# Performance work log

Measured on AMD Instinct MI355X. Metric: run time of the kernel, lower is better.

## Reference

```python
import jax, jax.numpy as jnp
import numpy as np

B, S, H, W, DF, D, HID, ITERS = 8, 8, 64, 64, 64, 64, 128, 3
EPS = 1e-8


def build_grid(h, w):
    ranges = [np.linspace(-1.0, 1.0, num=h), np.linspace(-1.0, 1.0, num=w)]
    g = np.meshgrid(*ranges, sparse=False, indexing='xy')
    return jnp.asarray(np.stack(g, axis=-1), dtype=jnp.float32)  # [H, W, 2]


def ln(x, g, b):
    m = jnp.mean(x, axis=-1, keepdims=True)
    v = jnp.mean((x - m) ** 2, axis=-1, keepdims=True)
    return (x - m) * jax.lax.rsqrt(v + 1e-5) * g + b


def setup_inputs() -> dict:
    key = jax.random.key(0)
    ks = iter(jax.random.split(key, 64))
    def nrm(shape, s=0.02):
        return jax.random.normal(next(ks), shape, jnp.float32) * s
    inp = {}
    inp['inputs'] = jax.random.normal(next(ks), (B, H, W, DF), jnp.float32)
    # learned slot inits and learned per-slot position / scale factors
    inp['slots_p'] = jax.random.normal(next(ks), (1, S, D), jnp.float32)
    inp['s_pos_p'] = 2.0 * jax.random.uniform(next(ks), (1, S, 2), jnp.float32) - 1.0
    inp['s_scale_p'] = 0.1 + 0.01 * jax.random.normal(next(ks), (1, S, 2), jnp.float32)
    # soft position embedding Linear(2, D)
    inp['W_pos'] = nrm((2, D)); inp['b_pos'] = jnp.zeros((D,), jnp.float32)
    # q/k/v projections
    inp['Wq'] = nrm((D, D)); inp['bq'] = jnp.zeros((D,), jnp.float32)
    inp['Wk'] = nrm((DF, D)); inp['bk'] = jnp.zeros((D,), jnp.float32)
    inp['Wv'] = nrm((DF, D)); inp['bv'] = jnp.zeros((D,), jnp.float32)
    # layernorms
    inp['g_in'] = jnp.ones((DF,), jnp.float32); inp['b_in'] = jnp.zeros((DF,), jnp.float32)
    inp['g_slots'] = jnp.ones((D,), jnp.float32); inp['b_slots'] = jnp.zeros((D,), jnp.float32)
    inp['g_k'] = jnp.ones((D,), jnp.float32); inp['b_k'] = jnp.zeros((D,), jnp.float32)
    inp['g_v'] = jnp.ones((D,), jnp.float32); inp['b_v'] = jnp.zeros((D,), jnp.float32)
    # shared kv MLP fc1_kv / fc2_kv
    inp['W1'] = nrm((D, 2 * D)); inp['b1'] = jnp.zeros((2 * D,), jnp.float32)
    inp['W2'] = nrm((2 * D, D)); inp['b2'] = jnp.zeros((D,), jnp.float32)
    # GRUCell (torch layout transposed to [in, 3*D])
    inp['W_ih'] = nrm((D, 3 * D)); inp['b_ih'] = jnp.zeros((3 * D,), jnp.float32)
    inp['W_hh'] = nrm((D, 3 * D)); inp['b_hh'] = jnp.zeros((3 * D,), jnp.float32)
    # residual slot MLP
    inp['g_pre'] = jnp.ones((D,), jnp.float32); inp['b_pre'] = jnp.zeros((D,), jnp.float32)
    inp['Wf1'] = nrm((D, HID)); inp['bf1'] = jnp.zeros((HID,), jnp.float32)
    inp['Wf2'] = nrm((HID, D)); inp['bf2'] = jnp.zeros((D,), jnp.float32)
    return inp


def reference(inputs, slots_p, s_pos_p, s_scale_p, W_pos, b_pos, Wq, bq, Wk, bk, Wv, bv,
              g_in, b_in, g_slots, b_slots, g_k, b_k, g_v, b_v, W1, b1, W2, b2,
              W_ih, W_hh, b_ih, b_hh, g_pre, b_pre, Wf1, bf1, Wf2, bf2):
    grid = build_grid(H, W)                 # [H, W, 2]
    grid_flat = grid.reshape(-1, 2)          # [HW, 2]
    scale = D ** (-0.5)

    x = ln(inputs, g_in, b_in)
    k0 = x @ Wk + bk                         # [B, H, W, D]
    v0 = x @ Wv + bv

    slots = jnp.broadcast_to(slots_p, (B, S, D))
    s_pos = jnp.clip(jnp.broadcast_to(s_pos_p, (B, S, 2)), -1.0, 1.0)[:, :, None, None, :]
    s_scale = jnp.clip(jnp.broadcast_to(s_scale_p, (B, S, 2)), 1e-3, 2.0)[:, :, None, None, :]

    def proj_kv(base, sp, ss, g, b):
        gr = (grid[None, None] - sp) / (ss * 5.0)      # [B, S, H, W, 2]
        pe = gr @ W_pos + b_pos                        # [B, S, H, W, D]
        t = (base[:, None] + pe).reshape(B, S, H * W, D)
        t = ln(t, g, b)
        return jax.nn.relu(t @ W1 + b1) @ W2 + b2      # [B, S, HW, D]

    for i in range(ITERS + 1):
        slots_prev = slots
        q = ln(slots, g_slots, b_slots) @ Wq + bq       # [B, S, D]
        kk = proj_kv(k0, s_pos, s_scale, g_k, b_k)
        vv = proj_kv(v0, s_pos, s_scale, g_v, b_v)
        dots = jnp.einsum('bid,bijd->bij', q, kk) * scale
        attn_mask = jax.nn.softmax(dots, axis=1) + EPS  # softmax over slot axis
        attn = attn_mask / jnp.sum(attn_mask, axis=-1, keepdims=True)
        updates = jnp.einsum('bijd,bij->bid', vv, attn)
        if i < ITERS:
            xg = updates.reshape(-1, D) @ W_ih + b_ih
            hg = slots_prev.reshape(-1, D) @ W_hh + b_hh
            ir, iz, inn = jnp.split(xg, 3, axis=-1)
            hr, hz, hn = jnp.split(hg, 3, axis=-1)
            r = jax.nn.sigmoid(ir + hr)
            z = jax.nn.sigmoid(iz + hz)
            n = jnp.tanh(inn + r * hn)
            slots = ((1.0 - z) * n + z * slots_prev.reshape(-1, D)).reshape(B, S, D)
            slots = slots + (jax.nn.relu(ln(slots, g_pre, b_pre) @ Wf1 + bf1) @ Wf2 + bf2)
        else:
            slots = slots_prev
        # update per-slot position / scale from the attention mask
        sp = jnp.einsum('bij,jd->bid', attn_mask, grid_flat) / jnp.sum(attn_mask, axis=-1, keepdims=True)
        diff = grid_flat[None, None] - sp[:, :, None]   # [B, S, HW, 2]
        am = attn_mask + 1e-8
        ss = jnp.sqrt(jnp.einsum('bij,bijd->bid', am, diff ** 2) / jnp.sum(am, axis=-1, keepdims=True))
        s_pos = sp[:, :, None, None, :]
        s_scale = jnp.clip(ss, 1e-3, 2.0)[:, :, None, None, :]
    return slots, s_pos, s_scale, attn_mask
```

## Files before the change

kernel.cpp:

```cpp
#include <hip/hip_runtime.h>
#include <math.h>

typedef __bf16 bf16_t;
typedef __bf16 bfrag __attribute__((ext_vector_type(8)));
typedef float ffrag __attribute__((ext_vector_type(4)));

__device__ __forceinline__ float wave_sum(float v) {
#pragma unroll
  for (int m = 32; m >= 1; m >>= 1) v += __shfl_xor(v, m, 64);
  return v;
}
__device__ __forceinline__ float lin_(int i) { return -1.f + (2.f * (float)i) / 63.f; }
__device__ __forceinline__ float bflo(unsigned u) { return __uint_as_float(u << 16); }
__device__ __forceinline__ float bfhi(unsigned u) { return __uint_as_float(u & 0xFFFF0000u); }

__device__ __forceinline__ void pass_type(
    const bf16_t xs[][72], bf16_t t0s[][72],
    const bf16_t WTl[][72], const bf16_t W1l[][72],
    const float* __restrict__ bias, const float* wpxs, const float* wpys,
    const float* bpvs, float* __restrict__ statsG, bf16_t* __restrict__ P0G,
    int j0, int wv, int lq, int ln15) {
  ffrag C[4] = {{0,0,0,0},{0,0,0,0},{0,0,0,0},{0,0,0,0}};
#pragma unroll
  for (int ks = 0; ks < 2; ++ks) {
    bfrag a = *(const bfrag*)&xs[wv * 16 + ln15][ks * 32 + lq * 8];
#pragma unroll
    for (int nt = 0; nt < 4; ++nt) {
      bfrag bb = *(const bfrag*)&WTl[nt * 16 + ln15][ks * 32 + lq * 8];
      C[nt] = __builtin_amdgcn_mfma_f32_16x16x32_bf16(a, bb, C[nt], 0, 0, 0);
    }
  }
  float kv[4][4];
  float st[5][4];
#pragma unroll
  for (int i = 0; i < 5; ++i)
#pragma unroll
    for (int rg = 0; rg < 4; ++rg) st[i][rg] = 0.f;
#pragma unroll
  for (int nt = 0; nt < 4; ++nt) {
    int n = nt * 16 + ln15;
    float bn = bias[n], pxw = wpxs[n], pyw = wpys[n], bpw = bpvs[n];
#pragma unroll
    for (int rg = 0; rg < 4; ++rg) {
      float v = C[nt][rg] + bn;
      kv[nt][rg] = v;
      st[0][rg] += v; st[1][rg] += v * v; st[2][rg] += v * pxw;
      st[3][rg] += v * pyw; st[4][rg] += v * bpw;
    }
  }
#pragma unroll
  for (int i = 0; i < 5; ++i)
#pragma unroll
    for (int rg = 0; rg < 4; ++rg) {
      float v = st[i][rg];
      v += __shfl_xor(v, 1, 64); v += __shfl_xor(v, 2, 64);
      v += __shfl_xor(v, 4, 64); v += __shfl_xor(v, 8, 64);
      st[i][rg] = v;
    }
  if (ln15 == 0) {
#pragma unroll
    for (int rg = 0; rg < 4; ++rg) {
      int j = j0 + wv * 16 + lq * 4 + rg;
#pragma unroll
      for (int i = 0; i < 5; ++i) statsG[j * 5 + i] = st[i][rg];
    }
  }
#pragma unroll
  for (int nt = 0; nt < 4; ++nt)
#pragma unroll
    for (int rg = 0; rg < 4; ++rg)
      t0s[wv * 16 + lq * 4 + rg][nt * 16 + ln15] = (bf16_t)kv[nt][rg];
  ffrag D[8] = {{0,0,0,0},{0,0,0,0},{0,0,0,0},{0,0,0,0},
                {0,0,0,0},{0,0,0,0},{0,0,0,0},{0,0,0,0}};
#pragma unroll
  for (int ks = 0; ks < 2; ++ks) {
    bfrag a = *(const bfrag*)&t0s[wv * 16 + ln15][ks * 32 + lq * 8];
#pragma unroll
    for (int nt = 0; nt < 8; ++nt) {
      bfrag bb = *(const bfrag*)&W1l[nt * 16 + ln15][ks * 32 + lq * 8];
      D[nt] = __builtin_amdgcn_mfma_f32_16x16x32_bf16(a, bb, D[nt], 0, 0, 0);
    }
  }
#pragma unroll
  for (int nt = 0; nt < 8; ++nt)
#pragma unroll
    for (int rg = 0; rg < 4; ++rg)
      P0G[(size_t)(j0 + wv * 16 + lq * 4 + rg) * 128 + nt * 16 + ln15] =
          (bf16_t)D[nt][rg];
}

__global__ __launch_bounds__(256) void k_pre(
    const float* __restrict__ inp, const float* __restrict__ g_in,
    const float* __restrict__ b_in, const float* __restrict__ bk,
    const float* __restrict__ bv, const float* __restrict__ Wk,
    const float* __restrict__ Wv, const float* __restrict__ W1,
    const float* __restrict__ g_k, const float* __restrict__ g_v,
    const float* __restrict__ W_pos, const float* __restrict__ b_pos,
    bf16_t* __restrict__ P0k, bf16_t* __restrict__ P0v,
    float* __restrict__ statsK, float* __restrict__ statsV,
    const float* __restrict__ slots_p, const float* __restrict__ g_slots,
    const float* __restrict__ b_slots, const float* __restrict__ Wq,
    const float* __restrict__ bq, const float* __restrict__ W2,
    const float* __restrict__ b2, float* __restrict__ w2qg,
    float* __restrict__ b2qg,
    const float* __restrict__ b_k, const float* __restrict__ b_v,
    const float* __restrict__ b1, const float* __restrict__ s_pos_p,
    const float* __restrict__ s_scale_p,
    float4* __restrict__ nckA, float* __restrict__ nckB,
    float4* __restrict__ ncvA, float* __restrict__ ncvB,
    float* __restrict__ possum, float* __restrict__ sposS,
    float* __restrict__ sscaleS, float* __restrict__ slotsS) {
  __shared__ bf16_t xs[64][72];
  __shared__ bf16_t t0s[64][72];
  __shared__ bf16_t WkTl[64][72];
  __shared__ bf16_t WvTl[64][72];
  __shared__ bf16_t W1kl[128][72];
  __shared__ bf16_t W1vl[128][72];
  __shared__ float wpxs[64], wpys[64], bpvs[64];
  const int tid = threadIdx.x;
  const int j0 = blockIdx.x * 64;
  for (int i = tid; i < 4096; i += 256) {
    int n = i & 63, d = i >> 6;
    WkTl[n][d] = (bf16_t)Wk[i];
    WvTl[n][d] = (bf16_t)Wv[i];
  }
  for (int i = tid; i < 8192; i += 256) {
    int n = i & 127, c = i >> 7;
    float w = W1[i];
    W1kl[n][c] = (bf16_t)(g_k[c] * w);
    W1vl[n][c] = (bf16_t)(g_v[c] * w);
  }
  if (tid < 64) { wpxs[tid] = W_pos[tid]; wpys[tid] = W_pos[64 + tid]; bpvs[tid] = b_pos[tid]; }
  {
    const int px = tid >> 2, cg = tid & 3;
    const float* rowp = inp + (size_t)(j0 + px) * 64 + cg * 16;
    float v[16];
    *(float4*)&v[0]  = ((const float4*)rowp)[0];
    *(float4*)&v[4]  = ((const float4*)rowp)[1];
    *(float4*)&v[8]  = ((const float4*)rowp)[2];
    *(float4*)&v[12] = ((const float4*)rowp)[3];
    float s = 0.f, s2 = 0.f;
#pragma unroll
    for (int i = 0; i < 16; ++i) { s += v[i]; s2 += v[i] * v[i]; }
    s += __shfl_xor(s, 1, 64); s += __shfl_xor(s, 2, 64);
    s2 += __shfl_xor(s2, 1, 64); s2 += __shfl_xor(s2, 2, 64);
    float m = s * 0.015625f;
    float r = rsqrtf(s2 * 0.015625f - m * m + 1e-5f);
    float g[16], bb[16];
    *(float4*)&g[0]  = ((const float4*)(g_in + cg * 16))[0];
    *(float4*)&g[4]  = ((const float4*)(g_in + cg * 16))[1];
    *(float4*)&g[8]  = ((const float4*)(g_in + cg * 16))[2];
    *(float4*)&g[12] = ((const float4*)(g_in + cg * 16))[3];
    *(float4*)&bb[0]  = ((const float4*)(b_in + cg * 16))[0];
    *(float4*)&bb[4]  = ((const float4*)(b_in + cg * 16))[1];
    *(float4*)&bb[8]  = ((const float4*)(b_in + cg * 16))[2];
    *(float4*)&bb[12] = ((const float4*)(b_in + cg * 16))[3];
#pragma unroll
    for (int e = 0; e < 8; ++e) {
      float x0 = (v[2 * e] - m) * r * g[2 * e] + bb[2 * e];
      float x1 = (v[2 * e + 1] - m) * r * g[2 * e + 1] + bb[2 * e + 1];
      union { unsigned u; bf16_t h[2]; } cv;
      cv.h[0] = (bf16_t)x0; cv.h[1] = (bf16_t)x1;
      *(unsigned*)&xs[px][cg * 16 + 2 * e] = cv.u;
    }
  }
  __syncthreads();
  const int wv = tid >> 6, lane = tid & 63, lq = lane >> 4, ln15 = lane & 15;
  pass_type(xs, t0s, WkTl, W1kl, bk, wpxs, wpys, bpvs, statsK, P0k, j0, wv, lq, ln15);
  __syncthreads();
  pass_type(xs, t0s, WvTl, W1vl, bv, wpxs, wpys, bpvs, statsV, P0v, j0, wv, lq, ln15);
  if (blockIdx.x < 64 && tid < 64) {
    int bs = blockIdx.x, d = tid;
    float v = slots_p[(bs & 7) * 64 + d];
    float m = wave_sum(v) * 0.015625f;
    float c = v - m;
    float var = wave_sum(c * c) * 0.015625f;
    float xn = c * rsqrtf(var + 1e-5f) * g_slots[d] + b_slots[d];
    float q = bq[d];
    for (int cc = 0; cc < 64; ++cc) q = fmaf(__shfl(xn, cc, 64), Wq[cc * 64 + d], q);
    float w0 = 0.f, w1 = 0.f;
    for (int cc = 0; cc < 64; ++cc) {
      float qc = __shfl(q, cc, 64);
      w0 = fmaf(W2[d * 64 + cc], qc, w0);
      w1 = fmaf(W2[(64 + d) * 64 + cc], qc, w1);
    }
    w2qg[bs * 128 + d] = w0;
    w2qg[bs * 128 + 64 + d] = w1;
    float p = wave_sum(b2[d] * q);
    if (d == 0) b2qg[bs] = p;
  }
  if (blockIdx.x == 508 && tid < 128) {
    int n = tid;
    float wx = 0, wy = 0, wb = 0, u = 0, sk = 0;
    for (int c = 0; c < 64; ++c) {
      float w = W1[c * 128 + n];
      float wf = g_k[c] * w;
      float px = W_pos[c], py = W_pos[64 + c], bp = b_pos[c];
      wx += px * wf; wy += py * wf; wb += bp * wf; sk += wf; u += b_k[c] * w;
    }
    nckA[n] = make_float4(wx, wy, wb, u + b1[n]); nckB[n] = sk;
  }
  if (blockIdx.x == 509 && tid < 128) {
    int n = tid;
    float wx = 0, wy = 0, wb = 0, u = 0, sv = 0;
    for (int c = 0; c < 64; ++c) {
      float w = W1[c * 128 + n];
      float wf = g_v[c] * w;
      float px = W_pos[c], py = W_pos[64 + c], bp = b_pos[c];
      wx += px * wf; wy += py * wf; wb += bp * wf; sv += wf; u += b_v[c] * w;
    }
    ncvA[n] = make_float4(wx, wy, wb, u + b1[n]); ncvB[n] = sv;
  }
  if (blockIdx.x == 510) {
    if (tid < 64) {
      float px = W_pos[tid], py = W_pos[64 + tid], bp = b_pos[tid];
      float s9[9] = {px, py, bp, px * px, py * py, bp * bp, px * py, px * bp, py * bp};
#pragma unroll
      for (int i = 0; i < 9; ++i) {
        float v = wave_sum(s9[i]);
        if (tid == 0) possum[i] = v;
      }
    }
    if (tid < 128) {
      sposS[tid] = fminf(fmaxf(s_pos_p[tid & 15], -1.f), 1.f);
      sscaleS[tid] = fminf(fmaxf(s_scale_p[tid & 15], 0.001f), 2.f);
    }
    for (int i = tid; i < 4096; i += 256) slotsS[i] = slots_p[i & 511];
  }
}

template <int LAST>
__global__ __launch_bounds__(256) void k_iter(
    const bf16_t* __restrict__ P0kg, const bf16_t* __restrict__ P0vg,
    const float* __restrict__ statsK, const float* __restrict__ statsV,
    const float4* __restrict__ nckA, const float* __restrict__ nckB,
    const float4* __restrict__ ncvA, const float* __restrict__ ncvB,
    const float* __restrict__ possum, const float* __restrict__ w2qg,
    const float* __restrict__ b2qg, const float* __restrict__ sposS,
    const float* __restrict__ sscaleS, float* __restrict__ momP,
    float* __restrict__ HsumP, float* __restrict__ outAttn) {
  __shared__ unsigned P0kl[64 * 65];
  __shared__ unsigned P0vl[64 * 65];
  __shared__ float4 nckAl[128];
  __shared__ float nckBl[128];
  __shared__ float w2qTl[128][8];
  __shared__ float4 scalV[64][9];
  __shared__ float attnS[64][10];
  __shared__ float HsumW[4][8][128];
  __shared__ float momAcc[8][5];
  const int tid = threadIdx.x;
  const int tile = blockIdx.x, b = blockIdx.y;
  const int jg0 = b * 4096 + tile * 64;
#pragma unroll
  for (int r = 0; r < 4; ++r) {
    int idx = tid + 256 * r;
    int row = idx >> 4, seg = idx & 15;
    uint4 v = ((const uint4*)P0kg)[(size_t)(jg0 + row) * 16 + seg];
    unsigned* dst = &P0kl[row * 65 + seg * 4];
    dst[0] = v.x; dst[1] = v.y; dst[2] = v.z; dst[3] = v.w;
    if (!LAST) {
      uint4 w = ((const uint4*)P0vg)[(size_t)(jg0 + row) * 16 + seg];
      unsigned* d2 = &P0vl[row * 65 + seg * 4];
      d2[0] = w.x; d2[1] = w.y; d2[2] = w.z; d2[3] = w.w;
    }
  }
  if (tid < 128) { nckAl[tid] = nckA[tid]; nckBl[tid] = nckB[tid]; }
#pragma unroll
  for (int r = 0; r < 4; ++r) {
    int idx = tid + 256 * r;
    int s = idx >> 7, n = idx & 127;
    w2qTl[n][s] = w2qg[(b * 8 + s) * 128 + n];
  }
  if (tid < 40) momAcc[tid / 5][tid % 5] = 0.f;
  float4 ncv0 = {0, 0, 0, 0}, ncv1 = {0, 0, 0, 0};
  float wsv0 = 0.f, wsv1 = 0.f;
  if (!LAST) {
    int l = tid & 63;
    ncv0 = ncvA[l]; ncv1 = ncvA[l + 64];
    wsv0 = ncvB[l]; wsv1 = ncvB[l + 64];
  }
  __syncthreads();

  const int px = tid >> 2, sp = tid & 3;
  const int jimg = tile * 64 + px;
  const float gx = lin_(jimg & 63), gy = lin_(jimg >> 6);
  const float Swx = possum[0], Swy = possum[1], Sbp = possum[2];
  const float Swx2 = possum[3], Swy2 = possum[4], Sbp2 = possum[5];
  const float Swxy = possum[6], Swxb = possum[7], Swyb = possum[8];
  float skA[5], svA[5];
#pragma unroll
  for (int i = 0; i < 5; ++i) {
    skA[i] = statsK[(size_t)(jg0 + px) * 5 + i];
    svA[i] = statsV[(size_t)(jg0 + px) * 5 + i];
  }
  float c1a[8], c2a[8], rKa[8], mrKa[8];
#pragma unroll
  for (int s = 0; s < 8; ++s) {
    int bs = b * 8 + s;
    float spx = sposS[bs * 2], spy = sposS[bs * 2 + 1];
    float rxx = 1.f / (sscaleS[bs * 2] * 5.f);
    float ryy = 1.f / (sscaleS[bs * 2 + 1] * 5.f);
    float c1 = (gx - spx) * rxx, c2 = (gy - spy) * ryy;
    float quad = c1 * c1 * Swx2 + c2 * c2 * Swy2 + Sbp2 +
                 2.f * (c1 * c2 * Swxy + c1 * Swxb + c2 * Swyb);
    float mK = (skA[0] + c1 * Swx + c2 * Swy + Sbp) * 0.015625f;
    float e2K = (skA[1] + 2.f * (c1 * skA[2] + c2 * skA[3] + skA[4]) + quad) * 0.015625f;
    float rK = rsqrtf(e2K - mK * mK + 1e-5f);
    c1a[s] = c1; c2a[s] = c2; rKa[s] = rK; mrKa[s] = mK * rK;
    if (!LAST && (s >> 1) == sp) {
      float mV = (svA[0] + c1 * Swx + c2 * Swy + Sbp) * 0.015625f;
      float e2V = (svA[1] + 2.f * (c1 * svA[2] + c2 * svA[3] + svA[4]) + quad) * 0.015625f;
      float rV = rsqrtf(e2V - mV * mV + 1e-5f);
      scalV[px][s] = make_float4(c1, c2, rV, mV * rV);
    }
  }
  float d8[8] = {0, 0, 0, 0, 0, 0, 0, 0};
#pragma unroll 4
  for (int i = 0; i < 16; ++i) {
    int k = sp * 16 + i;
    unsigned u = P0kl[px * 65 + k];
    float p0 = bflo(u), p1 = bfhi(u);
    float4 A0 = nckAl[2 * k], A1 = nckAl[2 * k + 1];
    float ws0 = nckBl[2 * k], ws1 = nckBl[2 * k + 1];
    float4 q0a = *(const float4*)&w2qTl[2 * k][0];
    float4 q0b = *(const float4*)&w2qTl[2 * k][4];
    float4 q1a = *(const float4*)&w2qTl[2 * k + 1][0];
    float4 q1b = *(const float4*)&w2qTl[2 * k + 1][4];
    float qq0[8] = {q0a.x, q0a.y, q0a.z, q0a.w, q0b.x, q0b.y, q0b.z, q0b.w};
    float qq1[8] = {q1a.x, q1a.y, q1a.z, q1a.w, q1b.x, q1b.y, q1b.z, q1b.w};
    float bm0 = p0 + A0.z, bm1 = p1 + A1.z;
#pragma unroll
    for (int s = 0; s < 8; ++s) {
      float z0 = bm0 + c1a[s] * A0.x + c2a[s] * A0.y;
      float h0 = fmaxf(fmaf(rKa[s], z0, fmaf(-mrKa[s], ws0, A0.w)), 0.f);
      d8[s] = fmaf(h0, qq0[s], d8[s]);
      float z1 = bm1 + c1a[s] * A1.x + c2a[s] * A1.y;
      float h1 = fmaxf(fmaf(rKa[s], z1, fmaf(-mrKa[s], ws1, A1.w)), 0.f);
      d8[s] = fmaf(h1, qq1[s], d8[s]);
    }
  }
#pragma unroll
  for (int s = 0; s < 8; ++s) {
    float v = d8[s];
    v += __shfl_xor(v, 1, 64);
    v += __shfl_xor(v, 2, 64);
    d8[s] = (v + b2qg[b * 8 + s]) * 0.125f;
  }
  float mx = d8[0];
#pragma unroll
  for (int s = 1; s < 8; ++s) mx = fmaxf(mx, d8[s]);
  float tt = 0.f;
  float e8[8];
#pragma unroll
  for (int s = 0; s < 8; ++s) { e8[s] = expf(d8[s] - mx); tt += e8[s]; }
  float inv = 1.f / tt;
#pragma unroll
  for (int s = 0; s < 8; ++s) e8[s] = e8[s] * inv + 1e-8f;
  float wa, wb;
  if (sp == 0) { wa = e8[0]; wb = e8[1]; }
  else if (sp == 1) { wa = e8[2]; wb = e8[3]; }
  else if (sp == 2) { wa = e8[4]; wb = e8[5]; }
  else { wa = e8[6]; wb = e8[7]; }
  *(float2*)&attnS[px][sp * 2] = make_float2(wa, wb);
  if (LAST) {
    outAttn[(size_t)(b * 8 + sp * 2) * 4096 + jimg] = wa;
    outAttn[(size_t)(b * 8 + sp * 2 + 1) * 4096 + jimg] = wb;
  }
  {
    float mm[10] = {wa, wa * gx, wa * gy, wa * gx * gx, wa * gy * gy,
                    wb, wb * gx, wb * gy, wb * gx * gx, wb * gy * gy};
#pragma unroll
    for (int i = 0; i < 10; ++i) {
      float v = mm[i];
      v += __shfl_xor(v, 4, 64); v += __shfl_xor(v, 8, 64);
      v += __shfl_xor(v, 16, 64); v += __shfl_xor(v, 32, 64);
      mm[i] = v;
    }
    if ((tid & 63) < 4) {
#pragma unroll
      for (int i = 0; i < 5; ++i) {
        atomicAdd(&momAcc[sp * 2][i], mm[i]);
        atomicAdd(&momAcc[sp * 2 + 1][i], mm[5 + i]);
      }
    }
  }
  __syncthreads();

  if (!LAST) {
    const int w = tid >> 6, l = tid & 63;
    float hacc[8][2];
#pragma unroll
    for (int s = 0; s < 8; ++s) { hacc[s][0] = 0.f; hacc[s][1] = 0.f; }
    const unsigned short* P16 = (const unsigned short*)P0vl;
#pragma unroll 2
    for (int i = 0; i < 16; ++i) {
      int j = w * 16 + i;
      float pv0 = __uint_as_float((unsigned)P16[j * 130 + l] << 16);
      float pv1 = __uint_as_float((unsigned)P16[j * 130 + 64 + l] << 16);
      float bm0 = pv0 + ncv0.z, bm1 = pv1 + ncv1.z;
#pragma unroll
      for (int s = 0; s < 8; ++s) {
        float4 sc = scalV[j][s];
        float aw = attnS[j][s];
        float z0 = bm0 + sc.x * ncv0.x + sc.y * ncv0.y;
        float h0 = fmaxf(fmaf(sc.z, z0, fmaf(-sc.w, wsv0, ncv0.w)), 0.f);
        hacc[s][0] = fmaf(aw, h0, hacc[s][0]);
        float z1 = bm1 + sc.x * ncv1.x + sc.y * ncv1.y;
        float h1 = fmaxf(fmaf(sc.z, z1, fmaf(-sc.w, wsv1, ncv1.w)), 0.f);
        hacc[s][1] = fmaf(aw, h1, hacc[s][1]);
      }
    }
#pragma unroll
    for (int s = 0; s < 8; ++s) {
      HsumW[w][s][l] = hacc[s][0];
      HsumW[w][s][l + 64] = hacc[s][1];
    }
    __syncthreads();
#pragma unroll
    for (int r = 0; r < 4; ++r) {
      int i = tid + 256 * r;
      int s = i >> 7, n = i & 127;
      float v = HsumW[0][s][n] + HsumW[1][s][n] + HsumW[2][s][n] + HsumW[3][s][n];
      HsumP[((size_t)(b * 8 + s) * 64 + tile) * 128 + n] = v;
    }
  }
  if (tid < 40)
    momP[((size_t)(b * 8 + tid / 5) * 64 + tile) * 5 + tid % 5] =
        momAcc[tid / 5][tid % 5];
}

__global__ __launch_bounds__(192) void k_fin(
    const float* __restrict__ momP, const float* __restrict__ HsumP,
    const float* __restrict__ W2, const float* __restrict__ b2,
    const float* __restrict__ W_ih, const float* __restrict__ b_ih,
    const float* __restrict__ W_hh, const float* __restrict__ b_hh,
    const float* __restrict__ g_pre, const float* __restrict__ b_pre,
    const float* __restrict__ Wf1, const float* __restrict__ bf1,
    const float* __restrict__ Wf2, const float* __restrict__ bf2,
    const float* __restrict__ g_slots, const float* __restrict__ b_slots,
    const float* __restrict__ Wq, const float* __restrict__ bq,
    float* __restrict__ slotsS, float* __restrict__ sposS, float* __restrict__ sscaleS,
    float* __restrict__ w2qg, float* __restrict__ b2qg,
    float* __restrict__ outSlots, float* __restrict__ outSpos,
    float* __restrict__ outSscale, int last) {
  const int bs = blockIdx.x;
  const int t = threadIdx.x;
  __shared__ float hsum_s[128], upd[64], sprev[64], xg[192], hg[192];
  __shared__ float snew[64], xpre[64], hf[128], sfin[64], xn[64], qsh[64];
  __shared__ float mom_s[5];
  if (t < 64) {
    const float* mp = momP + ((size_t)bs * 64 + t) * 5;
    float m0 = mp[0], m1 = mp[1], m2 = mp[2], m3 = mp[3], m4 = mp[4];
    m0 = wave_sum(m0); m1 = wave_sum(m1); m2 = wave_sum(m2);
    m3 = wave_sum(m3); m4 = wave_sum(m4);
    if (t == 0) { mom_s[0] = m0; mom_s[1] = m1; mom_s[2] = m2; mom_s[3] = m3; mom_s[4] = m4; }
    if (!last) sprev[t] = slotsS[bs * 64 + t];
  }
  if (!last && t >= 64) {
    int n = t - 64;
    const float* hp = HsumP + (size_t)bs * 8192 + n;
    float a = 0.f;
#pragma unroll 8
    for (int tile = 0; tile < 64; ++tile) a += hp[tile * 128];
    hsum_s[n] = a;
  }
  __syncthreads();
  const float M0 = mom_s[0];
  const float M1x = mom_s[1], M1y = mom_s[2];
  const float M2x = mom_s[3], M2y = mom_s[4];
  const float invM0 = 1.f / M0;
  const float spx = M1x * invM0, spy = M1y * invM0;
  const float M0a = M0 + 4096.f * 1e-8f;
  const float G2 = 1408.6772487f * 1e-8f;
  const float vx = (M2x + G2 - 2.f * spx * M1x + spx * spx * M0a) / M0a;
  const float vy = (M2y + G2 - 2.f * spy * M1y + spy * spy * M0a) / M0a;
  float ssx = sqrtf(fmaxf(vx, 0.f)), ssy = sqrtf(fmaxf(vy, 0.f));
  ssx = fminf(fmaxf(ssx, 0.001f), 2.f);
  ssy = fminf(fmaxf(ssy, 0.001f), 2.f);
  if (t == 0) {
    sposS[bs * 2 + 0] = spx; sposS[bs * 2 + 1] = spy;
    sscaleS[bs * 2 + 0] = ssx; sscaleS[bs * 2 + 1] = ssy;
    if (last) {
      outSpos[bs * 2 + 0] = spx; outSpos[bs * 2 + 1] = spy;
      outSscale[bs * 2 + 0] = ssx; outSscale[bs * 2 + 1] = ssy;
    }
  }
  if (last) {
    if (t < 64) outSlots[bs * 64 + t] = slotsS[bs * 64 + t];
    return;
  }
  if (t < 64) {
    float a = 0.f;
#pragma unroll
    for (int k = 0; k < 128; ++k) a += hsum_s[k] * W2[k * 64 + t];
    upd[t] = a * invM0 + b2[t];
  }
  __syncthreads();
  {
    float a = b_ih[t], h = b_hh[t];
#pragma unroll
    for (int d = 0; d < 64; ++d) {
      a += upd[d] * W_ih[d * 192 + t];
      h += sprev[d] * W_hh[d * 192 + t];
    }
    xg[t] = a; hg[t] = h;
  }
  __syncthreads();
  if (t < 64) {
    float r = 1.f / (1.f + expf(-(xg[t] + hg[t])));
    float z = 1.f / (1.f + expf(-(xg[64 + t] + hg[64 + t])));
    float n = tanhf(xg[128 + t] + r * hg[128 + t]);
    snew[t] = (1.f - z) * n + z * sprev[t];
  }
  __syncthreads();
  if (t < 64) {
    float v = snew[t];
    float m = wave_sum(v) * 0.015625f;
    float c = v - m;
    float var = wave_sum(c * c) * 0.015625f;
    xpre[t] = c * rsqrtf(var + 1e-5f) * g_pre[t] + b_pre[t];
  }
  __syncthreads();
  if (t < 128) {
    float a = bf1[t];
#pragma unroll
    for (int d = 0; d < 64; ++d) a += xpre[d] * Wf1[d * 128 + t];
    hf[t] = fmaxf(a, 0.f);
  }
  __syncthreads();
  if (t < 64) {
    float a = bf2[t];
#pragma unroll
    for (int k = 0; k < 128; ++k) a += hf[k] * Wf2[k * 64 + t];
    float nv = snew[t] + a;
    slotsS[bs * 64 + t] = nv;
    sfin[t] = nv;
  }
  __syncthreads();
  if (t < 64) {
    float v = sfin[t];
    float m = wave_sum(v) * 0.015625f;
    float c = v - m;
    float var = wave_sum(c * c) * 0.015625f;
    xn[t] = c * rsqrtf(var + 1e-5f) * g_slots[t] + b_slots[t];
  }
  __syncthreads();
  if (t < 64) {
    float a = bq[t];
#pragma unroll
    for (int d = 0; d < 64; ++d) a += xn[d] * Wq[d * 64 + t];
    qsh[t] = a;
  }
  __syncthreads();
  if (t < 128) {
    float a = 0.f;
#pragma unroll
    for (int d = 0; d < 64; ++d) a += W2[t * 64 + d] * qsh[d];
    w2qg[bs * 128 + t] = a;
  }
  if (t < 64) {
    float p = wave_sum(b2[t] * qsh[t]);
    if (t == 0) b2qg[bs] = p;
  }
}

extern "C" void kernel_launch(void* const* d_in, const int* in_sizes, int n_in,
                              void* d_out, int out_size, void* d_ws, size_t ws_size,
                              hipStream_t stream) {
  (void)in_sizes; (void)n_in; (void)out_size; (void)ws_size;
  const float* const* in = (const float* const*)d_in;
  float* ws = (float*)d_ws;
  bf16_t* P0k   = (bf16_t*)(ws + 0);
  bf16_t* P0v   = (bf16_t*)(ws + 2097152);
  float* statsK = ws + 4194304;
  float* statsV = ws + 4358144;
  float* w2qg   = ws + 4521984;
  float* b2qg   = ws + 4530176;
  float* slotsS = ws + 4530240;
  float* sposS  = ws + 4534336;
  float* sscaleS= ws + 4534464;
  float4* nckA  = (float4*)(ws + 4555392);
  float* nckB   = ws + 4555904;
  float4* ncvA  = (float4*)(ws + 4556032);
  float* ncvB   = ws + 4556544;
  float* possum = ws + 4556672;
  float* HsumP  = ws + 4560896;
  float* momP   = ws + 5085184;

  float* out = (float*)d_out;
  float* outSlots  = out;
  float* outSpos   = out + 4096;
  float* outSscale = out + 4224;
  float* outAttn   = out + 4352;

  k_pre<<<512, 256, 0, stream>>>(
      in[0], in[12], in[13], in[9], in[11], in[8], in[10], in[20], in[16], in[18],
      in[4], in[5], P0k, P0v, statsK, statsV,
      in[1], in[14], in[15], in[6], in[7], in[22], in[23], w2qg, b2qg,
      in[17], in[19], in[21], in[2], in[3],
      nckA, nckB, ncvA, ncvB, possum, sposS, sscaleS, slotsS);
  for (int i = 0; i < 4; ++i) {
    int last = (i == 3) ? 1 : 0;
    if (!last) {
      k_iter<0><<<dim3(64, 8), 256, 0, stream>>>(
          P0k, P0v, statsK, statsV, nckA, nckB, ncvA, ncvB, possum,
          w2qg, b2qg, sposS, sscaleS, momP, HsumP, outAttn);
    } else {
      k_iter<1><<<dim3(64, 8), 256, 0, stream>>>(
          P0k, P0v, statsK, statsV, nckA, nckB, ncvA, ncvB, possum,
          w2qg, b2qg, sposS, sscaleS, momP, HsumP, outAttn);
    }
    k_fin<<<64, 192, 0, stream>>>(momP, HsumP, in[22], in[23], in[24], in[25],
                                  in[26], in[27], in[28], in[29], in[30], in[31],
                                  in[32], in[33], in[14], in[15], in[6], in[7],
                                  slotsS, sposS, sscaleS, w2qg, b2qg,
                                  outSlots, outSpos, outSscale, last);
  }
}
```

Before: 287.1 us.

## Halve k_iter tile to 32 pixels, doubling blocks and per-pixel slot parallelism

k_iter now handles 32 pixels per block with 8 threads per pixel (one per slot) instead of 64 pixels with 4 threads, launching twice as many blocks. P0k rows are loaded straight into registers instead of through shared memory. The nckA, nckB and w2q constants are packed into one rotated shared table to cut bank conflicts. The value-aggregation phase writes per-tile partial sums directly without the cross-wave shared reduction, and k_fin reduces over twice as many partial tiles. The aim is more occupancy and less shared memory per block, at the cost of more partial-sum traffic and a larger final reduction.

```diff
diff --git a/kernel.cpp b/kernel.cpp
--- a/kernel.cpp
+++ b/kernel.cpp
@@ -230,7 +230,7 @@
 }
 
 template <int LAST>
-__global__ __launch_bounds__(256) void k_iter(
+__global__ __launch_bounds__(256, 4) void k_iter(
     const bf16_t* __restrict__ P0kg, const bf16_t* __restrict__ P0vg,
     const float* __restrict__ statsK, const float* __restrict__ statsV,
     const float4* __restrict__ nckA, const float* __restrict__ nckB,
@@ -239,60 +239,56 @@
     const float* __restrict__ b2qg, const float* __restrict__ sposS,
     const float* __restrict__ sscaleS, float* __restrict__ momP,
     float* __restrict__ HsumP, float* __restrict__ outAttn) {
-  __shared__ unsigned P0kl[64 * 65];
-  __shared__ unsigned P0vl[64 * 65];
-  __shared__ float4 nckAl[128];
-  __shared__ float nckBl[128];
-  __shared__ float w2qTl[128][8];
-  __shared__ float4 scalV[64][9];
-  __shared__ float attnS[64][10];
-  __shared__ float HsumW[4][8][128];
+  __shared__ unsigned P0vl[32 * 65];
+  __shared__ float ncqT[128 * 16];
+  __shared__ float4 scalV[32][9];
+  __shared__ float attnS[32][10];
   __shared__ float momAcc[8][5];
   const int tid = threadIdx.x;
   const int tile = blockIdx.x, b = blockIdx.y;
-  const int jg0 = b * 4096 + tile * 64;
-#pragma unroll
-  for (int r = 0; r < 4; ++r) {
-    int idx = tid + 256 * r;
-    int row = idx >> 4, seg = idx & 15;
-    uint4 v = ((const uint4*)P0kg)[(size_t)(jg0 + row) * 16 + seg];
-    unsigned* dst = &P0kl[row * 65 + seg * 4];
-    dst[0] = v.x; dst[1] = v.y; dst[2] = v.z; dst[3] = v.w;
-    if (!LAST) {
+  const int jg0 = b * 4096 + tile * 32;
+  const int px = tid >> 3, sp = tid & 7;
+  uint4 pk0 = ((const uint4*)P0kg)[(size_t)(jg0 + px) * 16 + sp * 2 + 0];
+  uint4 pk1 = ((const uint4*)P0kg)[(size_t)(jg0 + px) * 16 + sp * 2 + 1];
+  float skA[5], svA[5];
+#pragma unroll
+  for (int i = 0; i < 5; ++i) {
+    skA[i] = statsK[(size_t)(jg0 + px) * 5 + i];
+    if (!LAST) svA[i] = statsV[(size_t)(jg0 + px) * 5 + i];
+  }
+  if (!LAST) {
+#pragma unroll
+    for (int r = 0; r < 2; ++r) {
+      int idx = tid + 256 * r;
+      int row = idx >> 4, seg = idx & 15;
       uint4 w = ((const uint4*)P0vg)[(size_t)(jg0 + row) * 16 + seg];
       unsigned* d2 = &P0vl[row * 65 + seg * 4];
       d2[0] = w.x; d2[1] = w.y; d2[2] = w.z; d2[3] = w.w;
     }
   }
-  if (tid < 128) { nckAl[tid] = nckA[tid]; nckBl[tid] = nckB[tid]; }
-#pragma unroll
-  for (int r = 0; r < 4; ++r) {
-    int idx = tid + 256 * r;
-    int s = idx >> 7, n = idx & 127;
-    w2qTl[n][s] = w2qg[(b * 8 + s) * 128 + n];
+  {
+    int n = tid & 127, g = tid >> 7, r4 = ((n >> 4) & 3) * 4;
+    float* row = &ncqT[n * 16];
+    if (g == 0) {
+      float4 A = nckA[n];
+      row[(0 + r4) & 15] = A.x; row[(1 + r4) & 15] = A.y;
+      row[(2 + r4) & 15] = A.z; row[(3 + r4) & 15] = A.w;
+#pragma unroll
+      for (int s = 0; s < 4; ++s) row[(4 + s + r4) & 15] = w2qg[(b * 8 + s) * 128 + n];
+    } else {
+#pragma unroll
+      for (int s = 4; s < 8; ++s) row[(4 + s + r4) & 15] = w2qg[(b * 8 + s) * 128 + n];
+      row[(12 + r4) & 15] = nckB[n];
+    }
   }
   if (tid < 40) momAcc[tid / 5][tid % 5] = 0.f;
-  float4 ncv0 = {0, 0, 0, 0}, ncv1 = {0, 0, 0, 0};
-  float wsv0 = 0.f, wsv1 = 0.f;
-  if (!LAST) {
-    int l = tid & 63;
-    ncv0 = ncvA[l]; ncv1 = ncvA[l + 64];
-    wsv0 = ncvB[l]; wsv1 = ncvB[l + 64];
-  }
-  __syncthreads();
-
-  const int px = tid >> 2, sp = tid & 3;
-  const int jimg = tile * 64 + px;
+  __syncthreads();
+
+  const int jimg = tile * 32 + px;
   const float gx = lin_(jimg & 63), gy = lin_(jimg >> 6);
   const float Swx = possum[0], Swy = possum[1], Sbp = possum[2];
   const float Swx2 = possum[3], Swy2 = possum[4], Sbp2 = possum[5];
   const float Swxy = possum[6], Swxb = possum[7], Swyb = possum[8];
-  float skA[5], svA[5];
-#pragma unroll
-  for (int i = 0; i < 5; ++i) {
-    skA[i] = statsK[(size_t)(jg0 + px) * 5 + i];
-    svA[i] = statsV[(size_t)(jg0 + px) * 5 + i];
-  }
   float c1a[8], c2a[8], rKa[8], mrKa[8];
 #pragma unroll
   for (int s = 0; s < 8; ++s) {
@@ -307,27 +303,32 @@
     float e2K = (skA[1] + 2.f * (c1 * skA[2] + c2 * skA[3] + skA[4]) + quad) * 0.015625f;
     float rK = rsqrtf(e2K - mK * mK + 1e-5f);
     c1a[s] = c1; c2a[s] = c2; rKa[s] = rK; mrKa[s] = mK * rK;
-    if (!LAST && (s >> 1) == sp) {
+    if (!LAST && s == sp) {
       float mV = (svA[0] + c1 * Swx + c2 * Swy + Sbp) * 0.015625f;
       float e2V = (svA[1] + 2.f * (c1 * svA[2] + c2 * svA[3] + svA[4]) + quad) * 0.015625f;
       float rV = rsqrtf(e2V - mV * mV + 1e-5f);
       scalV[px][s] = make_float4(c1, c2, rV, mV * rV);
     }
   }
+  const unsigned uu[8] = {pk0.x, pk0.y, pk0.z, pk0.w, pk1.x, pk1.y, pk1.z, pk1.w};
+  const int r4 = (sp & 3) * 4;
   float d8[8] = {0, 0, 0, 0, 0, 0, 0, 0};
-#pragma unroll 4
-  for (int i = 0; i < 16; ++i) {
-    int k = sp * 16 + i;
-    unsigned u = P0kl[px * 65 + k];
-    float p0 = bflo(u), p1 = bfhi(u);
-    float4 A0 = nckAl[2 * k], A1 = nckAl[2 * k + 1];
-    float ws0 = nckBl[2 * k], ws1 = nckBl[2 * k + 1];
-    float4 q0a = *(const float4*)&w2qTl[2 * k][0];
-    float4 q0b = *(const float4*)&w2qTl[2 * k][4];
-    float4 q1a = *(const float4*)&w2qTl[2 * k + 1][0];
-    float4 q1b = *(const float4*)&w2qTl[2 * k + 1][4];
+#pragma unroll
+  for (int i = 0; i < 8; ++i) {
+    int n0 = 16 * sp + 2 * i;
+    const float* R0 = &ncqT[n0 * 16];
+    const float* R1 = R0 + 16;
+    float4 A0 = *(const float4*)&R0[r4];
+    float4 q0a = *(const float4*)&R0[(r4 + 4) & 15];
+    float4 q0b = *(const float4*)&R0[(r4 + 8) & 15];
+    float ws0 = R0[(r4 + 12) & 15];
+    float4 A1 = *(const float4*)&R1[r4];
+    float4 q1a = *(const float4*)&R1[(r4 + 4) & 15];
+    float4 q1b = *(const float4*)&R1[(r4 + 8) & 15];
+    float ws1 = R1[(r4 + 12) & 15];
     float qq0[8] = {q0a.x, q0a.y, q0a.z, q0a.w, q0b.x, q0b.y, q0b.z, q0b.w};
     float qq1[8] = {q1a.x, q1a.y, q1a.z, q1a.w, q1b.x, q1b.y, q1b.z, q1b.w};
+    float p0 = bflo(uu[i]), p1 = bfhi(uu[i]);
     float bm0 = p0 + A0.z, bm1 = p1 + A1.z;
 #pragma unroll
     for (int s = 0; s < 8; ++s) {
@@ -344,6 +345,7 @@
     float v = d8[s];
     v += __shfl_xor(v, 1, 64);
     v += __shfl_xor(v, 2, 64);
+    v += __shfl_xor(v, 4, 64);
     d8[s] = (v + b2qg[b * 8 + s]) * 0.125f;
   }
   float mx = d8[0];
@@ -356,77 +358,55 @@
   float inv = 1.f / tt;
 #pragma unroll
   for (int s = 0; s < 8; ++s) e8[s] = e8[s] * inv + 1e-8f;
-  float wa, wb;
-  if (sp == 0) { wa = e8[0]; wb = e8[1]; }
-  else if (sp == 1) { wa = e8[2]; wb = e8[3]; }
-  else if (sp == 2) { wa = e8[4]; wb = e8[5]; }
-  else { wa = e8[6]; wb = e8[7]; }
-  *(float2*)&attnS[px][sp * 2] = make_float2(wa, wb);
-  if (LAST) {
-    outAttn[(size_t)(b * 8 + sp * 2) * 4096 + jimg] = wa;
-    outAttn[(size_t)(b * 8 + sp * 2 + 1) * 4096 + jimg] = wb;
-  }
+  attnS[px][sp] = e8[sp];
+  if (LAST) outAttn[(size_t)(b * 8 + sp) * 4096 + jimg] = e8[sp];
   {
-    float mm[10] = {wa, wa * gx, wa * gy, wa * gx * gx, wa * gy * gy,
-                    wb, wb * gx, wb * gy, wb * gx * gx, wb * gy * gy};
-#pragma unroll
-    for (int i = 0; i < 10; ++i) {
+    float w = e8[sp];
+    float mm[5] = {w, w * gx, w * gy, w * gx * gx, w * gy * gy};
+#pragma unroll
+    for (int i = 0; i < 5; ++i) {
       float v = mm[i];
-      v += __shfl_xor(v, 4, 64); v += __shfl_xor(v, 8, 64);
-      v += __shfl_xor(v, 16, 64); v += __shfl_xor(v, 32, 64);
+      v += __shfl_xor(v, 8, 64); v += __shfl_xor(v, 16, 64);
+      v += __shfl_xor(v, 32, 64);
       mm[i] = v;
     }
-    if ((tid & 63) < 4) {
-#pragma unroll
-      for (int i = 0; i < 5; ++i) {
-        atomicAdd(&momAcc[sp * 2][i], mm[i]);
-        atomicAdd(&momAcc[sp * 2 + 1][i], mm[5 + i]);
-      }
-    }
-  }
-  __syncthreads();
+    if ((tid & 63) < 8) {
+#pragma unroll
+      for (int i = 0; i < 5; ++i) atomicAdd(&momAcc[sp][i], mm[i]);
+    }
+  }
+  __syncthreads();
+  if (tid < 40)
+    momP[((size_t)(b * 8 + tid / 5) * 128 + tile) * 5 + tid % 5] =
+        momAcc[tid / 5][tid % 5];
 
   if (!LAST) {
     const int w = tid >> 6, l = tid & 63;
-    float hacc[8][2];
-#pragma unroll
-    for (int s = 0; s < 8; ++s) { hacc[s][0] = 0.f; hacc[s][1] = 0.f; }
-    const unsigned short* P16 = (const unsigned short*)P0vl;
-#pragma unroll 2
-    for (int i = 0; i < 16; ++i) {
-      int j = w * 16 + i;
-      float pv0 = __uint_as_float((unsigned)P16[j * 130 + l] << 16);
-      float pv1 = __uint_as_float((unsigned)P16[j * 130 + 64 + l] << 16);
-      float bm0 = pv0 + ncv0.z, bm1 = pv1 + ncv1.z;
-#pragma unroll
-      for (int s = 0; s < 8; ++s) {
-        float4 sc = scalV[j][s];
-        float aw = attnS[j][s];
-        float z0 = bm0 + sc.x * ncv0.x + sc.y * ncv0.y;
-        float h0 = fmaxf(fmaf(sc.z, z0, fmaf(-sc.w, wsv0, ncv0.w)), 0.f);
-        hacc[s][0] = fmaf(aw, h0, hacc[s][0]);
-        float z1 = bm1 + sc.x * ncv1.x + sc.y * ncv1.y;
-        float h1 = fmaxf(fmaf(sc.z, z1, fmaf(-sc.w, wsv1, ncv1.w)), 0.f);
-        hacc[s][1] = fmaf(aw, h1, hacc[s][1]);
-      }
-    }
-#pragma unroll
-    for (int s = 0; s < 8; ++s) {
-      HsumW[w][s][l] = hacc[s][0];
-      HsumW[w][s][l + 64] = hacc[s][1];
-    }
-    __syncthreads();
-#pragma unroll
-    for (int r = 0; r < 4; ++r) {
-      int i = tid + 256 * r;
-      int s = i >> 7, n = i & 127;
-      float v = HsumW[0][s][n] + HsumW[1][s][n] + HsumW[2][s][n] + HsumW[3][s][n];
-      HsumP[((size_t)(b * 8 + s) * 64 + tile) * 128 + n] = v;
-    }
-  }
-  if (tid < 40)
-    momP[((size_t)(b * 8 + tid / 5) * 64 + tile) * 5 + tid % 5] =
-        momAcc[tid / 5][tid % 5];
+    const int s0 = 2 * w, s1 = 2 * w + 1;
+    float4 cv0 = ncvA[2 * l], cv1 = ncvA[2 * l + 1];
+    float wv0 = ncvB[2 * l], wv1 = ncvB[2 * l + 1];
+    float h00 = 0.f, h01 = 0.f, h10 = 0.f, h11 = 0.f;
+#pragma unroll 4
+    for (int j = 0; j < 32; ++j) {
+      unsigned u = P0vl[j * 65 + l];
+      float pv0 = bflo(u), pv1 = bfhi(u);
+      float bm0 = pv0 + cv0.z, bm1 = pv1 + cv1.z;
+      float4 sa = scalV[j][s0]; float aw = attnS[j][s0];
+      float z0 = bm0 + sa.x * cv0.x + sa.y * cv0.y;
+      h00 = fmaf(aw, fmaxf(fmaf(sa.z, z0, fmaf(-sa.w, wv0, cv0.w)), 0.f), h00);
+      float z1 = bm1 + sa.x * cv1.x + sa.y * cv1.y;
+      h01 = fmaf(aw, fmaxf(fmaf(sa.z, z1, fmaf(-sa.w, wv1, cv1.w)), 0.f), h01);
+      float4 sb = scalV[j][s1]; float ab = attnS[j][s1];
+      float z2 = bm0 + sb.x * cv0.x + sb.y * cv0.y;
+      h10 = fmaf(ab, fmaxf(fmaf(sb.z, z2, fmaf(-sb.w, wv0, cv0.w)), 0.f), h10);
+      float z3 = bm1 + sb.x * cv1.x + sb.y * cv1.y;
+      h11 = fmaf(ab, fmaxf(fmaf(sb.z, z3, fmaf(-sb.w, wv1, cv1.w)), 0.f), h11);
+    }
+    *(float2*)&HsumP[((size_t)(b * 8 + s0) * 128 + tile) * 128 + 2 * l] =
+        make_float2(h00, h01);
+    *(float2*)&HsumP[((size_t)(b * 8 + s1) * 128 + tile) * 128 + 2 * l] =
+        make_float2(h10, h11);
+  }
 }
 
 __global__ __launch_bounds__(192) void k_fin(
@@ -449,8 +429,9 @@
   __shared__ float snew[64], xpre[64], hf[128], sfin[64], xn[64], qsh[64];
   __shared__ float mom_s[5];
   if (t < 64) {
-    const float* mp = momP + ((size_t)bs * 64 + t) * 5;
-    float m0 = mp[0], m1 = mp[1], m2 = mp[2], m3 = mp[3], m4 = mp[4];
+    const float* mp = momP + ((size_t)bs * 128 + t) * 5;
+    float m0 = mp[0] + mp[320], m1 = mp[1] + mp[321], m2 = mp[2] + mp[322];
+    float m3 = mp[3] + mp[323], m4 = mp[4] + mp[324];
     m0 = wave_sum(m0); m1 = wave_sum(m1); m2 = wave_sum(m2);
     m3 = wave_sum(m3); m4 = wave_sum(m4);
     if (t == 0) { mom_s[0] = m0; mom_s[1] = m1; mom_s[2] = m2; mom_s[3] = m3; mom_s[4] = m4; }
@@ -458,10 +439,10 @@
   }
   if (!last && t >= 64) {
     int n = t - 64;
-    const float* hp = HsumP + (size_t)bs * 8192 + n;
+    const float* hp = HsumP + (size_t)bs * 16384 + n;
     float a = 0.f;
 #pragma unroll 8
-    for (int tile = 0; tile < 64; ++tile) a += hp[tile * 128];
+    for (int tile = 0; tile < 128; ++tile) a += hp[tile * 128];
     hsum_s[n] = a;
   }
   __syncthreads();
@@ -585,7 +566,7 @@
   float* ncvB   = ws + 4556544;
   float* possum = ws + 4556672;
   float* HsumP  = ws + 4560896;
-  float* momP   = ws + 5085184;
+  float* momP   = ws + 5609472;
 
   float* out = (float*)d_out;
   float* outSlots  = out;
@@ -602,11 +583,11 @@
   for (int i = 0; i < 4; ++i) {
     int last = (i == 3) ? 1 : 0;
     if (!last) {
-      k_iter<0><<<dim3(64, 8), 256, 0, stream>>>(
+      k_iter<0><<<dim3(128, 8), 256, 0, stream>>>(
           P0k, P0v, statsK, statsV, nckA, nckB, ncvA, ncvB, possum,
           w2qg, b2qg, sposS, sscaleS, momP, HsumP, outAttn);
     } else {
-      k_iter<1><<<dim3(64, 8), 256, 0, stream>>>(
+      k_iter<1><<<dim3(128, 8), 256, 0, stream>>>(
           P0k, P0v, statsK, statsV, nckA, nckB, ncvA, ncvB, possum,
           w2qg, b2qg, sposS, sscaleS, momP, HsumP, outAttn);
     }
```

New measurement: 269.1 us (median of 2 runs). -6.3%, faster.
